# Kernel tuning notes

Hardware: AMD Instinct MI355X
Metric: run time of the kernel (lower is better)

## Reference

```python
import jax, jax.numpy as jnp
import numpy as np

TILE = 128
NEG = -1e10


def rotate_half(x):
    half = x.shape[-1] // 2
    return jnp.concatenate([-x[..., half:], x[..., :half]], axis=-1)


def setup_inputs() -> dict:
    key = jax.random.key(0)
    ks = jax.random.split(key, 7)
    B, S, E, H, D, K = 1, 4096, 2048, 16, 128, 8
    T = S // TILE
    x = jax.random.normal(ks[0], (B, S, E), jnp.float32)
    wq = jax.random.normal(ks[1], (E, H * D), jnp.float32) * 0.02
    wk = jax.random.normal(ks[2], (E, H * D), jnp.float32) * 0.02
    wv = jax.random.normal(ks[3], (E, H * D), jnp.float32) * 0.02
    wo = jax.random.normal(ks[4], (H * D, E), jnp.float32) * 0.02
    rope_angles = jax.random.uniform(ks[5], (S, D // 2), jnp.float32)
    anchor_indices = jax.random.randint(ks[6], (B, H, T, K), 0, T).astype(jnp.int32)
    return {"x": x, "wq": wq, "wk": wk, "wv": wv, "wo": wo,
            "rope_angles": rope_angles, "anchor_indices": anchor_indices}


def reference(x, wq, wk, wv, wo, rope_angles, anchor_indices):
    B, S, E = x.shape
    D = rope_angles.shape[1] * 2          # head_dim
    H = wq.shape[1] // D                  # num_heads
    T = S // TILE                         # num_tiles
    sm_scale = 1.0 / jnp.sqrt(jnp.float32(D))

    # QKV projections -> [B, H, S, D]
    def proj(w):
        return (x @ w).reshape(B, S, H, D).transpose(0, 2, 1, 3).astype(jnp.float32)
    q, k, v = proj(wq), proj(wk), proj(wv)

    # RoPE (half-split / rotate_half format)
    cos = jnp.cos(rope_angles)[None, None]   # [1,1,S,D/2]
    sin = jnp.sin(rope_angles)[None, None]
    cos_f = jnp.concatenate([cos, cos], axis=-1)
    sin_f = jnp.concatenate([sin, sin], axis=-1)
    q = q * cos_f + rotate_half(q) * sin_f
    k = k * cos_f + rotate_half(k) * sin_f

    # Tile selection: anchor tiles + local (diagonal) tile -> [B,H,T,K+1]
    local = jnp.broadcast_to(jnp.arange(T, dtype=jnp.int32)[None, None, :, None], (B, H, T, 1))
    tile_sel = jnp.concatenate([anchor_indices, local], axis=-1)
    L = tile_sel.shape[-1] * TILE            # sparse_len
    token_idx = tile_sel[..., None] * TILE + jnp.arange(TILE, dtype=jnp.int32)[None, None, None, None, :]
    flat_idx = jnp.clip(token_idx.reshape(B, H, T, L), 0, S - 1)  # [B,H,T,L]

    # Gather selected KV tiles: [B,H,T,L,D]
    def gather(kv):
        return jnp.take_along_axis(kv, flat_idx.reshape(B, H, T * L, 1), axis=2).reshape(B, H, T, L, D)
    k_sp, v_sp = gather(k), gather(v)

    # Block-sparse attention per query tile
    q_t = q.reshape(B, H, T, TILE, D)
    logits = jnp.einsum('bhtqd,bhtkd->bhtqk', q_t, k_sp) * sm_scale
    q_pos = jnp.arange(S).reshape(T, TILE)
    future = flat_idx[:, :, :, None, :] > q_pos[None, None, :, :, None]  # causal mask on gathered keys
    logits = jnp.where(future, NEG, logits)
    w = jax.nn.softmax(logits, axis=-1)
    all_masked = jnp.all(future, axis=-1, keepdims=True)
    w = jnp.where(all_masked, 0.0, w)
    w = jnp.where(jnp.isnan(w), 0.0, w)
    out = jnp.einsum('bhtqk,bhtkd->bhtqd', w, v_sp)

    out = out.reshape(B, H, S, D).transpose(0, 2, 1, 3).reshape(B, S, H * D)
    return out @ wo
```

## Files before the change

kernel.cpp:

```cpp
#include <hip/hip_runtime.h>
#include <stdint.h>

typedef unsigned short u16;
typedef unsigned int u32;

#define S_LEN 4096
#define EMB 2048
#define NH 16
#define HD 128
#define HDTOT 2048
#define T_TILES 32
#define KANCH 8
#define SM_SCALE 0.088388347648318447f

typedef __bf16 bf16x8 __attribute__((ext_vector_type(8)));
typedef float f32x4 __attribute__((ext_vector_type(4)));

typedef const __attribute__((address_space(1))) u32 ga_u32;
typedef __attribute__((address_space(3))) u32 lds_u32;

__device__ __forceinline__ u16 f2bf(float f) {
  u32 b = __builtin_bit_cast(u32, f);
  b = (b + 0x7FFFu + ((b >> 16) & 1u)) >> 16;
  return (u16)b;
}
__device__ __forceinline__ float bf2f(u16 u) {
  return __builtin_bit_cast(float, ((u32)u) << 16);
}
__device__ __forceinline__ f32x4 mfma16(bf16x8 a, bf16x8 b, f32x4 c) {
  return __builtin_amdgcn_mfma_f32_16x16x32_bf16(a, b, c, 0, 0, 0);
}

#define ASM_LGKM0 do { asm volatile("s_waitcnt lgkmcnt(0)" ::: "memory"); \
                       __builtin_amdgcn_sched_barrier(0); } while (0)
#define ASM_VMC(n) do { asm volatile("s_waitcnt vmcnt(" #n ")" ::: "memory"); \
                        __builtin_amdgcn_sched_barrier(0); } while (0)

__global__ __launch_bounds__(256) void k_sincos(const float* __restrict__ ang,
                                                float2* __restrict__ tab) {
  int i = blockIdx.x * 256 + threadIdx.x;
  float a = ang[i];
  float s, c;
  __sincosf(a, &s, &c);
  tab[i] = make_float2(c, s);
}

__global__ __launch_bounds__(256) void k_convert_x(const float* __restrict__ x,
                                                   u16* __restrict__ xb) {
  int i = (blockIdx.x * 256 + threadIdx.x) * 4;
  float4 v = *(const float4*)(x + i);
  ushort4 o;
  o.x = f2bf(v.x); o.y = f2bf(v.y); o.z = f2bf(v.z); o.w = f2bf(v.w);
  *(ushort4*)(xb + i) = o;
}

__global__ __launch_bounds__(256) void k_transpose_w(
    const float* __restrict__ w0, const float* __restrict__ w1,
    const float* __restrict__ w2, const float* __restrict__ w3,
    u16* __restrict__ o0, u16* __restrict__ o1,
    u16* __restrict__ o2, u16* __restrict__ o3) {
  const float* w; u16* o;
  if (blockIdx.z == 0)      { w = w0; o = o0; }
  else if (blockIdx.z == 1) { w = w1; o = o1; }
  else if (blockIdx.z == 2) { w = w2; o = o2; }
  else                      { w = w3; o = o3; }
  __shared__ float tile[64][68];
  int n0 = blockIdx.x * 64, k0 = blockIdx.y * 64;
  int tid = threadIdx.x;
  int r = tid >> 4, cq = (tid & 15) << 2;
  for (int p = 0; p < 4; ++p) {
    float4 v = *(const float4*)(w + (size_t)(k0 + r + p * 16) * EMB + n0 + cq);
    tile[r + p * 16][cq + 0] = v.x;
    tile[r + p * 16][cq + 1] = v.y;
    tile[r + p * 16][cq + 2] = v.z;
    tile[r + p * 16][cq + 3] = v.w;
  }
  __syncthreads();
  for (int p = 0; p < 4; ++p) {
    int rn = r + p * 16;
    ushort4 u;
    u.x = f2bf(tile[cq + 0][rn]);
    u.y = f2bf(tile[cq + 1][rn]);
    u.z = f2bf(tile[cq + 2][rn]);
    u.w = f2bf(tile[cq + 3][rn]);
    *(ushort4*)(o + (size_t)(n0 + rn) * EMB + k0 + cq) = u;
  }
}

__global__ __launch_bounds__(256) void k_transpose_v(const u16* __restrict__ v,
                                                     u16* __restrict__ vt) {
  __shared__ u16 tile[64][72];
  int n0 = blockIdx.x * 64, s0 = blockIdx.y * 64;
  int tid = threadIdx.x;
  int r = tid >> 4, cq = (tid & 15) << 2;
  for (int p = 0; p < 4; ++p) {
    ushort4 u = *(const ushort4*)(v + (size_t)(s0 + r + p * 16) * HDTOT + n0 + cq);
    tile[r + p * 16][cq + 0] = u.x;
    tile[r + p * 16][cq + 1] = u.y;
    tile[r + p * 16][cq + 2] = u.z;
    tile[r + p * 16][cq + 3] = u.w;
  }
  __syncthreads();
  for (int p = 0; p < 4; ++p) {
    int rn = r + p * 16;
    ushort4 o;
    o.x = tile[cq + 0][rn];
    o.y = tile[cq + 1][rn];
    o.z = tile[cq + 2][rn];
    o.w = tile[cq + 3][rn];
    *(ushort4*)(vt + (size_t)(n0 + rn) * S_LEN + s0 + cq) = o;
  }
}

template <bool BF16OUT>
__device__ __forceinline__ void gemm_body(const u16* __restrict__ A,
                                          const u16* __restrict__ Bt,
                                          void* __restrict__ Cv,
                                          int N, int K, int m0, int n0,
                                          u16* As, u16* Bs) {
  const int tid = threadIdx.x;
  const int lane = tid & 63, wave = tid >> 6;
  const int quad = lane >> 4, l16 = lane & 15;
  const int wm = (wave >> 1) * 64, wn = (wave & 1) * 64;
  f32x4 acc[4][4] = {};

  const int flat0 = wave * 1024 + lane * 16;
  for (int kt = 0; kt < K; kt += 32) {
    for (int half = 0; half < 2; ++half) {
      int flat = flat0 + half * 4096;
      int row = flat >> 6, colb = flat & 63;
      const char* ga = (const char*)A + ((size_t)(m0 + row) * K + kt) * 2 + colb;
      const char* gb = (const char*)Bt + ((size_t)(n0 + row) * K + kt) * 2 + colb;
      int loff = wave * 1024 + half * 4096;
      __builtin_amdgcn_global_load_lds((ga_u32*)ga, (lds_u32*)((char*)As + loff), 16, 0, 0);
      __builtin_amdgcn_global_load_lds((ga_u32*)gb, (lds_u32*)((char*)Bs + loff), 16, 0, 0);
    }
    __syncthreads();
    bf16x8 af[4], bfr[4];
    for (int mt = 0; mt < 4; ++mt)
      af[mt] = *(const bf16x8*)(As + (wm + mt * 16 + l16) * 32 + quad * 8);
    for (int nt = 0; nt < 4; ++nt)
      bfr[nt] = *(const bf16x8*)(Bs + (wn + nt * 16 + l16) * 32 + quad * 8);
    for (int mt = 0; mt < 4; ++mt)
      for (int nt = 0; nt < 4; ++nt)
        acc[mt][nt] = mfma16(af[mt], bfr[nt], acc[mt][nt]);
    __syncthreads();
  }
  for (int mt = 0; mt < 4; ++mt) {
    int row = m0 + wm + mt * 16 + quad * 4;
    for (int nt = 0; nt < 4; ++nt) {
      int col = n0 + wn + nt * 16 + l16;
      for (int r = 0; r < 4; ++r) {
        if (BF16OUT)
          ((u16*)Cv)[(size_t)(row + r) * N + col] = f2bf(acc[mt][nt][r]);
        else
          ((float*)Cv)[(size_t)(row + r) * N + col] = acc[mt][nt][r];
      }
    }
  }
}

template <bool BF16OUT>
__global__ __launch_bounds__(256) void k_gemm(const u16* __restrict__ A,
                                              const u16* __restrict__ Bt,
                                              void* __restrict__ Cv,
                                              int N, int K) {
  __shared__ __align__(16) u16 As[128 * 32];
  __shared__ __align__(16) u16 Bs[128 * 32];
  gemm_body<BF16OUT>(A, Bt, Cv, N, K, blockIdx.y * 128, blockIdx.x * 128, As, Bs);
}

__global__ __launch_bounds__(512, 2) void k_gemm256_qkv(
    const u16* __restrict__ A, const u16* __restrict__ Bt,
    u16* __restrict__ q, u16* __restrict__ k, u16* __restrict__ v,
    const float2* __restrict__ cssn) {
  __shared__ __align__(16) u16 lds[65536];
  int flat = blockIdx.y * 24 + blockIdx.x;
  flat = (flat & 7) * 48 + (flat >> 3);
  const int bx = flat % 24, by = flat / 24;
  const int m0 = by * 256;
  const int n0g = bx * 256;
  u16* out = (bx < 8) ? q : ((bx < 16) ? k : v);
  const int ncol0 = (bx & 7) * 256;

  const int tid = threadIdx.x;
  const int lane = tid & 63, wave = tid >> 6;
  const int quad = lane >> 4, l16 = lane & 15;
  const int wm = wave >> 2, wn = wave & 3;
  const int sw0 = (quad ^ (l16 & 7)) * 8, sw1 = ((quad ^ (l16 & 7)) ^ 4) * 8;

  size_t soff[2];
#pragma unroll
  for (int p = 0; p < 2; ++p) {
    int fl = p * 8192 + tid * 16;
    int row = fl >> 7;
    int gsw = ((fl >> 4) & 7) ^ (row & 7);
    soff[p] = (size_t)row * 4096 + (size_t)(gsw * 16);
  }
  const char* aBase = (const char*)A + (size_t)m0 * 4096;
  const char* bBase = (const char*)Bt + (size_t)n0g * 4096;
  const int dstW = wave * 1024;

  auto stA = [&](int buf, int half, int kt) {
#pragma unroll
    for (int p = 0; p < 2; ++p)
      __builtin_amdgcn_global_load_lds(
          (ga_u32*)(aBase + (size_t)half * 524288 + (size_t)kt * 128 + soff[p]),
          (lds_u32*)((char*)lds + buf * 32768 + half * 16384 + p * 8192 + dstW),
          16, 0, 0);
  };
  auto stB = [&](int buf, int half, int kt) {
#pragma unroll
    for (int p = 0; p < 2; ++p)
      __builtin_amdgcn_global_load_lds(
          (ga_u32*)(bBase + (size_t)half * 524288 + (size_t)kt * 128 + soff[p]),
          (lds_u32*)((char*)lds + 65536 + buf * 32768 + half * 16384 + p * 8192 + dstW),
          16, 0, 0);
  };
  const u16* aRd = lds + wm * 8192 + l16 * 64;
  const u16* bRd = lds + 32768 + (wn * 16 + l16) * 64;

  f32x4 acc[8][4] = {};

  stB(0, 0, 0); stA(0, 0, 0); stB(0, 1, 0); stA(0, 1, 0);
  stB(1, 0, 1); stA(1, 0, 1);
  ASM_VMC(4);
  __builtin_amdgcn_s_barrier();

  const int NT = EMB / 64;
  for (int j = 0; j < NT; ++j) {
    const int par = j & 1;
    const u16* aT = aRd + par * 16384;
    const u16* bT = bRd + par * 16384;
    bf16x8 af[4][2], blo[2][2], bhi[2][2];
#pragma unroll
    for (int m = 0; m < 4; ++m) {
      af[m][0] = *(const bf16x8*)(aT + m * 1024 + sw0);
      af[m][1] = *(const bf16x8*)(aT + m * 1024 + sw1);
    }
#pragma unroll
    for (int n = 0; n < 2; ++n) {
      blo[n][0] = *(const bf16x8*)(bT + n * 4096 + sw0);
      blo[n][1] = *(const bf16x8*)(bT + n * 4096 + sw1);
    }
    if (j + 1 < NT) stB(1 - par, 1, j + 1);
    __builtin_amdgcn_s_barrier();
    ASM_LGKM0;
    __builtin_amdgcn_s_setprio(1);
#pragma unroll
    for (int m = 0; m < 4; ++m)
#pragma unroll
      for (int n = 0; n < 2; ++n) {
        acc[m][n] = mfma16(af[m][0], blo[n][0], acc[m][n]);
        acc[m][n] = mfma16(af[m][1], blo[n][1], acc[m][n]);
      }
    __builtin_amdgcn_s_setprio(0);
    __builtin_amdgcn_s_barrier();
#pragma unroll
    for (int n = 0; n < 2; ++n) {
      bhi[n][0] = *(const bf16x8*)(bT + (n + 2) * 4096 + sw0);
      bhi[n][1] = *(const bf16x8*)(bT + (n + 2) * 4096 + sw1);
    }
    if (j + 1 < NT) stA(1 - par, 1, j + 1);
    __builtin_amdgcn_s_barrier();
    ASM_LGKM0;
    __builtin_amdgcn_s_setprio(1);
#pragma unroll
    for (int m = 0; m < 4; ++m)
#pragma unroll
      for (int n = 0; n < 2; ++n) {
        acc[m][n + 2] = mfma16(af[m][0], bhi[n][0], acc[m][n + 2]);
        acc[m][n + 2] = mfma16(af[m][1], bhi[n][1], acc[m][n + 2]);
      }
    __builtin_amdgcn_s_setprio(0);
    __builtin_amdgcn_s_barrier();
#pragma unroll
    for (int m = 0; m < 4; ++m) {
      af[m][0] = *(const bf16x8*)(aT + (m + 4) * 1024 + sw0);
      af[m][1] = *(const bf16x8*)(aT + (m + 4) * 1024 + sw1);
    }
    if (j + 2 < NT) stB(par, 0, j + 2);
    __builtin_amdgcn_s_barrier();
    ASM_LGKM0;
    __builtin_amdgcn_s_setprio(1);
#pragma unroll
    for (int m = 0; m < 4; ++m)
#pragma unroll
      for (int n = 0; n < 2; ++n) {
        acc[m + 4][n + 2] = mfma16(af[m][0], bhi[n][0], acc[m + 4][n + 2]);
        acc[m + 4][n + 2] = mfma16(af[m][1], bhi[n][1], acc[m + 4][n + 2]);
      }
    __builtin_amdgcn_s_setprio(0);
    __builtin_amdgcn_s_barrier();
    if (j + 2 < NT) stA(par, 0, j + 2);
    __builtin_amdgcn_s_barrier();
    __builtin_amdgcn_s_setprio(1);
#pragma unroll
    for (int m = 0; m < 4; ++m)
#pragma unroll
      for (int n = 0; n < 2; ++n) {
        acc[m + 4][n] = mfma16(af[m][0], blo[n][0], acc[m + 4][n]);
        acc[m + 4][n] = mfma16(af[m][1], blo[n][1], acc[m + 4][n]);
      }
    __builtin_amdgcn_s_setprio(0);
    if (j == NT - 2) { ASM_VMC(0); } else { ASM_VMC(4); }
    __builtin_amdgcn_s_barrier();
  }

  if (bx < 16) {
    const int dcol = wn * 16 + l16;
#pragma unroll
    for (int m = 0; m < 8; ++m) {
      int srow = m0 + wm * 128 + m * 16 + quad * 4;
#pragma unroll
      for (int r = 0; r < 4; ++r) {
        int s = srow + r;
        float2 cs2 = cssn[s * 64 + dcol];
        u16* op = out + (size_t)s * HDTOT + ncol0 + dcol;
        float lo0 = acc[m][0][r], hi0 = acc[m][1][r];
        op[0]   = f2bf(lo0 * cs2.x - hi0 * cs2.y);
        op[64]  = f2bf(hi0 * cs2.x + lo0 * cs2.y);
        float lo1 = acc[m][2][r], hi1 = acc[m][3][r];
        op[128] = f2bf(lo1 * cs2.x - hi1 * cs2.y);
        op[192] = f2bf(hi1 * cs2.x + lo1 * cs2.y);
      }
    }
  } else {
#pragma unroll
    for (int m = 0; m < 8; ++m) {
      int row = m0 + wm * 128 + m * 16 + quad * 4;
#pragma unroll
      for (int n = 0; n < 4; ++n) {
        int col = ncol0 + (wn + 4 * n) * 16 + l16;
#pragma unroll
        for (int r = 0; r < 4; ++r)
          out[(size_t)(row + r) * HDTOT + col] = f2bf(acc[m][n][r]);
      }
    }
  }
}

__device__ __forceinline__ bf16x8 ldsfrag(const u16* __restrict__ sbuf, int r, int cb) {
  return *(const bf16x8*)(sbuf + r * 128 + (((cb ^ (r & 15)) << 3)));
}
__device__ __forceinline__ bf16x8 ldsfragV(const u16* __restrict__ sbuf, int r, int cb) {
  return *(const bf16x8*)(sbuf + r * 64 + (((cb ^ (r & 7)) << 3)));
}

__global__ __launch_bounds__(512, 4) void k_attn(const u16* __restrict__ q,
                                                 const u16* __restrict__ k,
                                                 const u16* __restrict__ vt,
                                                 const int* __restrict__ anch,
                                                 u16* __restrict__ out) {
  __shared__ __align__(16) u16 bufK[2][64 * 128];
  __shared__ __align__(16) u16 bufV[2][128 * 64];
  __shared__ int s_tj[KANCH + 1];
  __shared__ int s_nv;
  const int i = blockIdx.x;
  const int p2 = (i ^ (i >> 8)) & 1;
  const int c = i >> 1;
  const int t = p2 ? (15 - (c >> 4)) : (16 + (c >> 4));
  const int h = c & 15;
  const int tid = threadIdx.x;
  const int lane = tid & 63, wave = tid >> 6;
  const int quad = lane >> 4, l16 = lane & 15;
  const int wq0 = wave * 16;

  int offK[2], offV[2];
#pragma unroll
  for (int p = 0; p < 2; ++p) {
    int krow = (wave * 2 + p) * 4 + (lane >> 4);
    int kcol = ((lane & 15) ^ (krow & 15)) << 3;
    offK[p] = (krow * HDTOT + kcol) * 2;
    int vrow = (wave * 2 + p) * 8 + (lane >> 3);
    int vcol = ((lane & 7) ^ (vrow & 7)) << 3;
    offV[p] = (vrow * S_LEN + vcol) * 2;
  }

  if (tid == 0) {
    int nv = 0;
    for (int j = 0; j < KANCH; ++j) {
      int tj = anch[((h * T_TILES) + t) * KANCH + j];
      if (tj <= t) s_tj[nv++] = tj;
    }
    s_tj[nv++] = t;
    s_nv = nv;
  }

  {
    const char* gq = (const char*)(q + (size_t)(t * 128) * HDTOT + h * HD);
    char* lq = (char*)bufK + wave * 4096;
#pragma unroll
    for (int p = 0; p < 4; ++p) {
      int qrow = (wave * 4 + p) * 4 + (lane >> 4);
      int qcol = ((lane & 15) ^ (qrow & 15)) << 3;
      __builtin_amdgcn_global_load_lds((ga_u32*)(gq + (qrow * HDTOT + qcol) * 2),
                                       (lds_u32*)(lq + p * 1024), 16, 0, 0);
    }
  }
  __syncthreads();

  bf16x8 qf[4];
#pragma unroll
  for (int ks = 0; ks < 4; ++ks)
    qf[ks] = ldsfrag(&bufK[0][0], wq0 + l16, ks * 4 + quad);

  const int nv2 = 2 * s_nv;
  const char* kh = (const char*)(k + h * HD);
  const char* vh = (const char*)(vt + (size_t)(h * HD) * S_LEN);

  __syncthreads();

  {
    int key0 = s_tj[0] * 128;
    const char* gk = kh + (size_t)key0 * (HDTOT * 2);
    const char* gv = vh + (size_t)key0 * 2;
    char* lk = (char*)bufK[0] + wave * 2048;
    char* lv = (char*)bufV[0] + wave * 2048;
#pragma unroll
    for (int p = 0; p < 2; ++p) {
      __builtin_amdgcn_global_load_lds((ga_u32*)(gk + offK[p]),
                                       (lds_u32*)(lk + p * 1024), 16, 0, 0);
      __builtin_amdgcn_global_load_lds((ga_u32*)(gv + offV[p]),
                                       (lds_u32*)(lv + p * 1024), 16, 0, 0);
    }
  }

  f32x4 oacc[8] = {};
  float m_st = -1e30f, l_st = 0.f;

  for (int it = 0; it < nv2; ++it) {
    const int par = it & 1;
    const u16* K_c = bufK[par];
    const u16* V_c = bufV[par];
    const int tj = s_tj[it >> 1];
    const int half = it & 1;
    const bool diag = (tj == t);

    __syncthreads();

    if (it + 1 < nv2) {
      int inx = it + 1;
      int key0 = s_tj[inx >> 1] * 128 + (inx & 1) * 64;
      const char* gk = kh + (size_t)key0 * (HDTOT * 2);
      const char* gv = vh + (size_t)key0 * 2;
      char* lk = (char*)bufK[1 - par] + wave * 2048;
      char* lv = (char*)bufV[1 - par] + wave * 2048;
#pragma unroll
      for (int p = 0; p < 2; ++p) {
        __builtin_amdgcn_global_load_lds((ga_u32*)(gk + offK[p]),
                                         (lds_u32*)(lk + p * 1024), 16, 0, 0);
        __builtin_amdgcn_global_load_lds((ga_u32*)(gv + offV[p]),
                                         (lds_u32*)(lv + p * 1024), 16, 0, 0);
      }
    }

    f32x4 sacc[4] = {};
#pragma unroll
    for (int ks = 0; ks < 4; ++ks)
#pragma unroll
      for (int a = 0; a < 4; ++a) {
        bf16x8 kf = ldsfrag(K_c, a * 16 + l16, ks * 4 + quad);
        sacc[a] = mfma16(kf, qf[ks], sacc[a]);
      }

    u32 pl[4], ph[4];
    float alpha;
    {
      const int qr = wq0 + l16;
      const int kb = half * 64;
      float rmax = -1e30f;
#pragma unroll
      for (int a = 0; a < 4; ++a) {
        f32x4 s4 = sacc[a];
#pragma unroll
        for (int r = 0; r < 4; ++r) {
          float sv = s4[r] * SM_SCALE;
          if (diag && (kb + a * 16 + quad * 4 + r > qr)) sv = -1e30f;
          s4[r] = sv;
          rmax = fmaxf(rmax, sv);
        }
        sacc[a] = s4;
      }
      rmax = fmaxf(rmax, __shfl_xor(rmax, 16));
      rmax = fmaxf(rmax, __shfl_xor(rmax, 32));
      float mnew = fmaxf(m_st, rmax);
      alpha = __expf(m_st - mnew);
      m_st = mnew;
      float rsum = 0.f;
#pragma unroll
      for (int a = 0; a < 4; ++a) {
        f32x4 s4 = sacc[a];
        float p0 = __expf(s4[0] - mnew);
        float p1 = __expf(s4[1] - mnew);
        float p2 = __expf(s4[2] - mnew);
        float p3 = __expf(s4[3] - mnew);
        rsum += (p0 + p1) + (p2 + p3);
        pl[a] = __builtin_amdgcn_perm(__builtin_bit_cast(u32, p1) + 0x8000u,
                                      __builtin_bit_cast(u32, p0) + 0x8000u,
                                      0x07060302u);
        ph[a] = __builtin_amdgcn_perm(__builtin_bit_cast(u32, p3) + 0x8000u,
                                      __builtin_bit_cast(u32, p2) + 0x8000u,
                                      0x07060302u);
      }
      rsum += __shfl_xor(rsum, 16);
      rsum += __shfl_xor(rsum, 32);
      l_st = l_st * alpha + rsum;
    }

    {
      f32x4 av;
#pragma unroll
      for (int r = 0; r < 4; ++r)
        av[r] = __shfl(alpha, (lane & 48) | (quad * 4 + r));
#pragma unroll
      for (int nt = 0; nt < 8; ++nt) {
        f32x4 o4 = oacc[nt];
        o4[0] *= av[0]; o4[1] *= av[1]; o4[2] *= av[2]; o4[3] *= av[3];
        oacc[nt] = o4;
      }
    }

    const int srcA = ((quad & 1) << 5) + l16;
    const int srcB = srcA + 16;
    const int hi = quad >> 1;
#pragma unroll
    for (int cc = 0; cc < 2; ++cc) {
      u32 x0 = __shfl(pl[2 * cc], srcA), x1 = __shfl(ph[2 * cc], srcA);
      u32 x2 = __shfl(pl[2 * cc], srcB), x3 = __shfl(ph[2 * cc], srcB);
      u32 y0 = __shfl(pl[2 * cc + 1], srcA), y1 = __shfl(ph[2 * cc + 1], srcA);
      u32 y2 = __shfl(pl[2 * cc + 1], srcB), y3 = __shfl(ph[2 * cc + 1], srcB);
      uint4 w;
      w.x = hi ? y0 : x0;
      w.y = hi ? y1 : x1;
      w.z = hi ? y2 : x2;
      w.w = hi ? y3 : x3;
      bf16x8 pa = __builtin_bit_cast(bf16x8, w);
#pragma unroll
      for (int nt = 0; nt < 8; ++nt) {
        bf16x8 vf = ldsfragV(V_c, nt * 16 + l16, cc * 4 + quad);
        oacc[nt] = mfma16(pa, vf, oacc[nt]);
      }
    }
  }

  {
    float linv = 1.0f / l_st;
    f32x4 iv;
#pragma unroll
    for (int r = 0; r < 4; ++r)
      iv[r] = __shfl(linv, (lane & 48) | (quad * 4 + r));
#pragma unroll
    for (int r = 0; r < 4; ++r) {
      size_t srow_o = (size_t)(t * 128 + wq0 + quad * 4 + r);
#pragma unroll
      for (int nt = 0; nt < 8; ++nt)
        out[srow_o * HDTOT + h * HD + nt * 16 + l16] = f2bf(oacc[nt][r] * iv[r]);
    }
  }
}

extern "C" void kernel_launch(void* const* d_in, const int* in_sizes, int n_in,
                              void* d_out, int out_size, void* d_ws, size_t ws_size,
                              hipStream_t stream) {
  const float* x   = (const float*)d_in[0];
  const float* wq  = (const float*)d_in[1];
  const float* wk  = (const float*)d_in[2];
  const float* wv  = (const float*)d_in[3];
  const float* wo  = (const float*)d_in[4];
  const float* ang = (const float*)d_in[5];
  const int* anch  = (const int*)d_in[6];

  char* ws = (char*)d_ws;
  const size_t SZ_SE = (size_t)S_LEN * HDTOT * sizeof(u16);
  const size_t SZ_W  = (size_t)EMB * EMB * sizeof(u16);
  u16* xb   = (u16*)(ws);
  u16* qb   = (u16*)(ws + SZ_SE);
  u16* kb   = (u16*)(ws + 2 * SZ_SE);
  u16* vb   = (u16*)(ws + 3 * SZ_SE);
  u16* vtb  = (u16*)(ws + 4 * SZ_SE);
  u16* attn = (u16*)(ws + 5 * SZ_SE);
  u16* wqT  = (u16*)(ws + 6 * SZ_SE);
  u16* wkT  = (u16*)(ws + 6 * SZ_SE + SZ_W);
  u16* wvT  = (u16*)(ws + 6 * SZ_SE + 2 * SZ_W);
  u16* woT  = (u16*)(ws + 6 * SZ_SE + 3 * SZ_W);

  float2* cssn = (float2*)d_out;

  k_sincos<<<1024, 256, 0, stream>>>(ang, cssn);
  k_convert_x<<<8192, 256, 0, stream>>>(x, xb);
  k_transpose_w<<<dim3(32, 32, 4), 256, 0, stream>>>(wq, wk, wv, wo, wqT, wkT, wvT, woT);
  k_gemm256_qkv<<<dim3(24, 16), 512, 0, stream>>>(xb, wqT, qb, kb, vb, cssn);
  k_transpose_v<<<dim3(32, 64), 256, 0, stream>>>(vb, vtb);
  k_attn<<<dim3(512), 512, 0, stream>>>(qb, kb, vtb, anch, attn);
  k_gemm<false><<<dim3(16, 32), 256, 0, stream>>>(attn, woT, d_out, EMB, HDTOT);
}
```

Measured before the change: 382.2 us.

## Shrink QKV GEMM tile to 128x256 with K-step 32 and higher occupancy

After: 389.3 us. No clear change (+1.9%).

```diff
diff --git a/kernel.cpp b/kernel.cpp
--- a/kernel.cpp
+++ b/kernel.cpp
@@ -170,15 +170,15 @@
   gemm_body<BF16OUT>(A, Bt, Cv, N, K, blockIdx.y * 128, blockIdx.x * 128, As, Bs);
 }
 
-__global__ __launch_bounds__(512, 2) void k_gemm256_qkv(
+__global__ __launch_bounds__(512, 4) void k_gemm_qkv128(
     const u16* __restrict__ A, const u16* __restrict__ Bt,
     u16* __restrict__ q, u16* __restrict__ k, u16* __restrict__ v,
     const float2* __restrict__ cssn) {
-  __shared__ __align__(16) u16 lds[65536];
+  __shared__ __align__(16) u16 lds[24576];
   int flat = blockIdx.y * 24 + blockIdx.x;
-  flat = (flat & 7) * 48 + (flat >> 3);
+  flat = (flat & 7) * 96 + (flat >> 3);
   const int bx = flat % 24, by = flat / 24;
-  const int m0 = by * 256;
+  const int m0 = by * 128;
   const int n0g = bx * 256;
   u16* out = (bx < 8) ? q : ((bx < 16) ? k : v);
   const int ncol0 = (bx & 7) * 256;
@@ -187,131 +187,82 @@
   const int lane = tid & 63, wave = tid >> 6;
   const int quad = lane >> 4, l16 = lane & 15;
   const int wm = wave >> 2, wn = wave & 3;
-  const int sw0 = (quad ^ (l16 & 7)) * 8, sw1 = ((quad ^ (l16 & 7)) ^ 4) * 8;
-
-  size_t soff[2];
-#pragma unroll
-  for (int p = 0; p < 2; ++p) {
-    int fl = p * 8192 + tid * 16;
-    int row = fl >> 7;
-    int gsw = ((fl >> 4) & 7) ^ (row & 7);
-    soff[p] = (size_t)row * 4096 + (size_t)(gsw * 16);
+  const int sw = (quad ^ (l16 & 3)) * 8;
+
+  u32 soffA, soffB1;
+  {
+    int r = tid >> 2, g = tid & 3;
+    soffA = (u32)r * 4096 + (u32)((g ^ (r & 3)) * 16);
+    int r1 = 128 + r;
+    soffB1 = (u32)r1 * 4096 + (u32)((g ^ (r1 & 3)) * 16);
   }
   const char* aBase = (const char*)A + (size_t)m0 * 4096;
   const char* bBase = (const char*)Bt + (size_t)n0g * 4096;
   const int dstW = wave * 1024;
 
-  auto stA = [&](int buf, int half, int kt) {
-#pragma unroll
-    for (int p = 0; p < 2; ++p)
-      __builtin_amdgcn_global_load_lds(
-          (ga_u32*)(aBase + (size_t)half * 524288 + (size_t)kt * 128 + soff[p]),
-          (lds_u32*)((char*)lds + buf * 32768 + half * 16384 + p * 8192 + dstW),
-          16, 0, 0);
+  auto stA = [&](int buf, int kt) {
+    __builtin_amdgcn_global_load_lds(
+        (ga_u32*)(aBase + (size_t)kt * 64 + soffA),
+        (lds_u32*)((char*)lds + buf * 8192 + dstW), 16, 0, 0);
   };
-  auto stB = [&](int buf, int half, int kt) {
-#pragma unroll
-    for (int p = 0; p < 2; ++p)
-      __builtin_amdgcn_global_load_lds(
-          (ga_u32*)(bBase + (size_t)half * 524288 + (size_t)kt * 128 + soff[p]),
-          (lds_u32*)((char*)lds + 65536 + buf * 32768 + half * 16384 + p * 8192 + dstW),
-          16, 0, 0);
+  auto stB = [&](int buf, int kt) {
+    __builtin_amdgcn_global_load_lds(
+        (ga_u32*)(bBase + (size_t)kt * 64 + soffA),
+        (lds_u32*)((char*)lds + 16384 + buf * 16384 + dstW), 16, 0, 0);
+    __builtin_amdgcn_global_load_lds(
+        (ga_u32*)(bBase + (size_t)kt * 64 + soffB1),
+        (lds_u32*)((char*)lds + 16384 + buf * 16384 + 8192 + dstW), 16, 0, 0);
   };
-  const u16* aRd = lds + wm * 8192 + l16 * 64;
-  const u16* bRd = lds + 32768 + (wn * 16 + l16) * 64;
-
-  f32x4 acc[8][4] = {};
-
-  stB(0, 0, 0); stA(0, 0, 0); stB(0, 1, 0); stA(0, 1, 0);
-  stB(1, 0, 1); stA(1, 0, 1);
-  ASM_VMC(4);
+
+  const int aOff = (wm * 64 + l16) * 32 + sw;
+  const int bOff = (wn * 16 + l16) * 32 + sw;
+
+  f32x4 acc[4][4] = {};
+
+  stA(0, 0); stB(0, 0);
+  stA(1, 1); stB(1, 1);
+  ASM_VMC(3);
   __builtin_amdgcn_s_barrier();
 
-  const int NT = EMB / 64;
+  const int NT = EMB / 32;
   for (int j = 0; j < NT; ++j) {
     const int par = j & 1;
-    const u16* aT = aRd + par * 16384;
-    const u16* bT = bRd + par * 16384;
-    bf16x8 af[4][2], blo[2][2], bhi[2][2];
-#pragma unroll
-    for (int m = 0; m < 4; ++m) {
-      af[m][0] = *(const bf16x8*)(aT + m * 1024 + sw0);
-      af[m][1] = *(const bf16x8*)(aT + m * 1024 + sw1);
-    }
-#pragma unroll
-    for (int n = 0; n < 2; ++n) {
-      blo[n][0] = *(const bf16x8*)(bT + n * 4096 + sw0);
-      blo[n][1] = *(const bf16x8*)(bT + n * 4096 + sw1);
-    }
-    if (j + 1 < NT) stB(1 - par, 1, j + 1);
-    __builtin_amdgcn_s_barrier();
+    const u16* aT = lds + par * 4096 + aOff;
+    const u16* bT = lds + 8192 + par * 8192 + bOff;
+    bf16x8 af[4], bfr[4];
+#pragma unroll
+    for (int m = 0; m < 4; ++m)
+      af[m] = *(const bf16x8*)(aT + m * 512);
+#pragma unroll
+    for (int n = 0; n < 4; ++n)
+      bfr[n] = *(const bf16x8*)(bT + n * 2048);
     ASM_LGKM0;
     __builtin_amdgcn_s_setprio(1);
 #pragma unroll
-    for (int m = 0; m < 4; ++m)
-#pragma unroll
-      for (int n = 0; n < 2; ++n) {
-        acc[m][n] = mfma16(af[m][0], blo[n][0], acc[m][n]);
-        acc[m][n] = mfma16(af[m][1], blo[n][1], acc[m][n]);
-      }
+    for (int m = 0; m < 4; ++m) {
+      acc[m][0] = mfma16(af[m], bfr[0], acc[m][0]);
+      acc[m][1] = mfma16(af[m], bfr[1], acc[m][1]);
+    }
     __builtin_amdgcn_s_setprio(0);
     __builtin_amdgcn_s_barrier();
-#pragma unroll
-    for (int n = 0; n < 2; ++n) {
-      bhi[n][0] = *(const bf16x8*)(bT + (n + 2) * 4096 + sw0);
-      bhi[n][1] = *(const bf16x8*)(bT + (n + 2) * 4096 + sw1);
-    }
-    if (j + 1 < NT) stA(1 - par, 1, j + 1);
-    __builtin_amdgcn_s_barrier();
-    ASM_LGKM0;
+    if (j + 2 < NT) { stA(par, j + 2); stB(par, j + 2); }
     __builtin_amdgcn_s_setprio(1);
 #pragma unroll
-    for (int m = 0; m < 4; ++m)
-#pragma unroll
-      for (int n = 0; n < 2; ++n) {
-        acc[m][n + 2] = mfma16(af[m][0], bhi[n][0], acc[m][n + 2]);
-        acc[m][n + 2] = mfma16(af[m][1], bhi[n][1], acc[m][n + 2]);
-      }
+    for (int m = 0; m < 4; ++m) {
+      acc[m][2] = mfma16(af[m], bfr[2], acc[m][2]);
+      acc[m][3] = mfma16(af[m], bfr[3], acc[m][3]);
+    }
     __builtin_amdgcn_s_setprio(0);
-    __builtin_amdgcn_s_barrier();
-#pragma unroll
-    for (int m = 0; m < 4; ++m) {
-      af[m][0] = *(const bf16x8*)(aT + (m + 4) * 1024 + sw0);
-      af[m][1] = *(const bf16x8*)(aT + (m + 4) * 1024 + sw1);
-    }
-    if (j + 2 < NT) stB(par, 0, j + 2);
-    __builtin_amdgcn_s_barrier();
-    ASM_LGKM0;
-    __builtin_amdgcn_s_setprio(1);
-#pragma unroll
-    for (int m = 0; m < 4; ++m)
-#pragma unroll
-      for (int n = 0; n < 2; ++n) {
-        acc[m + 4][n + 2] = mfma16(af[m][0], bhi[n][0], acc[m + 4][n + 2]);
-        acc[m + 4][n + 2] = mfma16(af[m][1], bhi[n][1], acc[m + 4][n + 2]);
-      }
-    __builtin_amdgcn_s_setprio(0);
-    __builtin_amdgcn_s_barrier();
-    if (j + 2 < NT) stA(par, 0, j + 2);
-    __builtin_amdgcn_s_barrier();
-    __builtin_amdgcn_s_setprio(1);
-#pragma unroll
-    for (int m = 0; m < 4; ++m)
-#pragma unroll
-      for (int n = 0; n < 2; ++n) {
-        acc[m + 4][n] = mfma16(af[m][0], blo[n][0], acc[m + 4][n]);
-        acc[m + 4][n] = mfma16(af[m][1], blo[n][1], acc[m + 4][n]);
-      }
-    __builtin_amdgcn_s_setprio(0);
-    if (j == NT - 2) { ASM_VMC(0); } else { ASM_VMC(4); }
-    __builtin_amdgcn_s_barrier();
+    if (j < NT - 2) { ASM_VMC(3); }
+    else if (j == NT - 2) { ASM_VMC(0); }
+    if (j < NT - 1) __builtin_amdgcn_s_barrier();
   }
 
   if (bx < 16) {
     const int dcol = wn * 16 + l16;
 #pragma unroll
-    for (int m = 0; m < 8; ++m) {
-      int srow = m0 + wm * 128 + m * 16 + quad * 4;
+    for (int m = 0; m < 4; ++m) {
+      int srow = m0 + wm * 64 + m * 16 + quad * 4;
 #pragma unroll
       for (int r = 0; r < 4; ++r) {
         int s = srow + r;
@@ -327,8 +278,8 @@
     }
   } else {
 #pragma unroll
-    for (int m = 0; m < 8; ++m) {
-      int row = m0 + wm * 128 + m * 16 + quad * 4;
+    for (int m = 0; m < 4; ++m) {
+      int row = m0 + wm * 64 + m * 16 + quad * 4;
 #pragma unroll
       for (int n = 0; n < 4; ++n) {
         int col = ncol0 + (wn + 4 * n) * 16 + l16;
@@ -590,7 +541,7 @@
   k_sincos<<<1024, 256, 0, stream>>>(ang, cssn);
   k_convert_x<<<8192, 256, 0, stream>>>(x, xb);
   k_transpose_w<<<dim3(32, 32, 4), 256, 0, stream>>>(wq, wk, wv, wo, wqT, wkT, wvT, woT);
-  k_gemm256_qkv<<<dim3(24, 16), 512, 0, stream>>>(xb, wqT, qb, kb, vb, cssn);
+  k_gemm_qkv128<<<dim3(24, 32), 512, 0, stream>>>(xb, wqT, qb, kb, vb, cssn);
   k_transpose_v<<<dim3(32, 64), 256, 0, stream>>>(vb, vtb);
   k_attn<<<dim3(512), 512, 0, stream>>>(qb, kb, vtb, anch, attn);
   k_gemm<false><<<dim3(16, 32), 256, 0, stream>>>(attn, woT, d_out, EMB, HDTOT);
```

## Process two query sub-tiles per wave in attention and swizzle GEMM LDS

Applied to the files above, without the earlier changes.

Result: no change. 382.5 us (+0.1%).

```diff
diff --git a/kernel.cpp b/kernel.cpp
--- a/kernel.cpp
+++ b/kernel.cpp
@@ -122,13 +122,16 @@
   const int lane = tid & 63, wave = tid >> 6;
   const int quad = lane >> 4, l16 = lane & 15;
   const int wm = (wave >> 1) * 64, wn = (wave & 1) * 64;
+  const int sw = (quad ^ (l16 & 3) ^ ((l16 >> 2) & 3)) * 8;
   f32x4 acc[4][4] = {};
 
   const int flat0 = wave * 1024 + lane * 16;
   for (int kt = 0; kt < K; kt += 32) {
     for (int half = 0; half < 2; ++half) {
       int flat = flat0 + half * 4096;
-      int row = flat >> 6, colb = flat & 63;
+      int row = flat >> 6;
+      int gl = (flat >> 4) & 3;
+      int colb = ((gl ^ (row & 3) ^ ((row >> 2) & 3)) << 4);
       const char* ga = (const char*)A + ((size_t)(m0 + row) * K + kt) * 2 + colb;
       const char* gb = (const char*)Bt + ((size_t)(n0 + row) * K + kt) * 2 + colb;
       int loff = wave * 1024 + half * 4096;
@@ -138,9 +141,9 @@
     __syncthreads();
     bf16x8 af[4], bfr[4];
     for (int mt = 0; mt < 4; ++mt)
-      af[mt] = *(const bf16x8*)(As + (wm + mt * 16 + l16) * 32 + quad * 8);
+      af[mt] = *(const bf16x8*)(As + (wm + mt * 16 + l16) * 32 + sw);
     for (int nt = 0; nt < 4; ++nt)
-      bfr[nt] = *(const bf16x8*)(Bs + (wn + nt * 16 + l16) * 32 + quad * 8);
+      bfr[nt] = *(const bf16x8*)(Bs + (wn + nt * 16 + l16) * 32 + sw);
     for (int mt = 0; mt < 4; ++mt)
       for (int nt = 0; nt < 4; ++nt)
         acc[mt][nt] = mfma16(af[mt], bfr[nt], acc[mt][nt]);
@@ -347,7 +350,7 @@
   return *(const bf16x8*)(sbuf + r * 64 + (((cb ^ (r & 7)) << 3)));
 }
 
-__global__ __launch_bounds__(512, 4) void k_attn(const u16* __restrict__ q,
+__global__ __launch_bounds__(256, 2) void k_attn(const u16* __restrict__ q,
                                                  const u16* __restrict__ k,
                                                  const u16* __restrict__ vt,
                                                  const int* __restrict__ anch,
@@ -364,15 +367,15 @@
   const int tid = threadIdx.x;
   const int lane = tid & 63, wave = tid >> 6;
   const int quad = lane >> 4, l16 = lane & 15;
-  const int wq0 = wave * 16;
-
-  int offK[2], offV[2];
-#pragma unroll
-  for (int p = 0; p < 2; ++p) {
-    int krow = (wave * 2 + p) * 4 + (lane >> 4);
+  const int wq0 = wave * 32;
+
+  int offK[4], offV[4];
+#pragma unroll
+  for (int p = 0; p < 4; ++p) {
+    int krow = (wave * 4 + p) * 4 + (lane >> 4);
     int kcol = ((lane & 15) ^ (krow & 15)) << 3;
     offK[p] = (krow * HDTOT + kcol) * 2;
-    int vrow = (wave * 2 + p) * 8 + (lane >> 3);
+    int vrow = (wave * 4 + p) * 8 + (lane >> 3);
     int vcol = ((lane & 7) ^ (vrow & 7)) << 3;
     offV[p] = (vrow * S_LEN + vcol) * 2;
   }
@@ -389,10 +392,10 @@
 
   {
     const char* gq = (const char*)(q + (size_t)(t * 128) * HDTOT + h * HD);
-    char* lq = (char*)bufK + wave * 4096;
-#pragma unroll
-    for (int p = 0; p < 4; ++p) {
-      int qrow = (wave * 4 + p) * 4 + (lane >> 4);
+    char* lq = (char*)bufK + wave * 8192;
+#pragma unroll
+    for (int p = 0; p < 8; ++p) {
+      int qrow = (wave * 8 + p) * 4 + (lane >> 4);
       int qcol = ((lane & 15) ^ (qrow & 15)) << 3;
       __builtin_amdgcn_global_load_lds((ga_u32*)(gq + (qrow * HDTOT + qcol) * 2),
                                        (lds_u32*)(lq + p * 1024), 16, 0, 0);
@@ -400,10 +403,12 @@
   }
   __syncthreads();
 
-  bf16x8 qf[4];
-#pragma unroll
-  for (int ks = 0; ks < 4; ++ks)
-    qf[ks] = ldsfrag(&bufK[0][0], wq0 + l16, ks * 4 + quad);
+  bf16x8 qf[2][4];
+#pragma unroll
+  for (int qh = 0; qh < 2; ++qh)
+#pragma unroll
+    for (int ks = 0; ks < 4; ++ks)
+      qf[qh][ks] = ldsfrag(&bufK[0][0], wq0 + qh * 16 + l16, ks * 4 + quad);
 
   const int nv2 = 2 * s_nv;
   const char* kh = (const char*)(k + h * HD);
@@ -415,10 +420,10 @@
     int key0 = s_tj[0] * 128;
     const char* gk = kh + (size_t)key0 * (HDTOT * 2);
     const char* gv = vh + (size_t)key0 * 2;
-    char* lk = (char*)bufK[0] + wave * 2048;
-    char* lv = (char*)bufV[0] + wave * 2048;
-#pragma unroll
-    for (int p = 0; p < 2; ++p) {
+    char* lk = (char*)bufK[0] + wave * 4096;
+    char* lv = (char*)bufV[0] + wave * 4096;
+#pragma unroll
+    for (int p = 0; p < 4; ++p) {
       __builtin_amdgcn_global_load_lds((ga_u32*)(gk + offK[p]),
                                        (lds_u32*)(lk + p * 1024), 16, 0, 0);
       __builtin_amdgcn_global_load_lds((ga_u32*)(gv + offV[p]),
@@ -426,8 +431,9 @@
     }
   }
 
-  f32x4 oacc[8] = {};
-  float m_st = -1e30f, l_st = 0.f;
+  f32x4 oacc[2][8] = {};
+  float m_st[2] = {-1e30f, -1e30f};
+  float l_st[2] = {0.f, 0.f};
 
   for (int it = 0; it < nv2; ++it) {
     const int par = it & 1;
@@ -444,10 +450,10 @@
       int key0 = s_tj[inx >> 1] * 128 + (inx & 1) * 64;
       const char* gk = kh + (size_t)key0 * (HDTOT * 2);
       const char* gv = vh + (size_t)key0 * 2;
-      char* lk = (char*)bufK[1 - par] + wave * 2048;
-      char* lv = (char*)bufV[1 - par] + wave * 2048;
-#pragma unroll
-      for (int p = 0; p < 2; ++p) {
+      char* lk = (char*)bufK[1 - par] + wave * 4096;
+      char* lv = (char*)bufV[1 - par] + wave * 4096;
+#pragma unroll
+      for (int p = 0; p < 4; ++p) {
         __builtin_amdgcn_global_load_lds((ga_u32*)(gk + offK[p]),
                                          (lds_u32*)(lk + p * 1024), 16, 0, 0);
         __builtin_amdgcn_global_load_lds((ga_u32*)(gv + offV[p]),
@@ -455,24 +461,28 @@
       }
     }
 
-    f32x4 sacc[4] = {};
+    f32x4 sacc[2][4] = {};
+    __builtin_amdgcn_s_setprio(1);
 #pragma unroll
     for (int ks = 0; ks < 4; ++ks)
 #pragma unroll
       for (int a = 0; a < 4; ++a) {
         bf16x8 kf = ldsfrag(K_c, a * 16 + l16, ks * 4 + quad);
-        sacc[a] = mfma16(kf, qf[ks], sacc[a]);
-      }
-
-    u32 pl[4], ph[4];
-    float alpha;
-    {
-      const int qr = wq0 + l16;
+        sacc[0][a] = mfma16(kf, qf[0][ks], sacc[0][a]);
+        sacc[1][a] = mfma16(kf, qf[1][ks], sacc[1][a]);
+      }
+    __builtin_amdgcn_s_setprio(0);
+
+    u32 pl[2][4], ph[2][4];
+    float alpha[2];
+#pragma unroll
+    for (int qh = 0; qh < 2; ++qh) {
+      const int qr = wq0 + qh * 16 + l16;
       const int kb = half * 64;
       float rmax = -1e30f;
 #pragma unroll
       for (int a = 0; a < 4; ++a) {
-        f32x4 s4 = sacc[a];
+        f32x4 s4 = sacc[qh][a];
 #pragma unroll
         for (int r = 0; r < 4; ++r) {
           float sv = s4[r] * SM_SCALE;
@@ -480,44 +490,45 @@
           s4[r] = sv;
           rmax = fmaxf(rmax, sv);
         }
-        sacc[a] = s4;
+        sacc[qh][a] = s4;
       }
       rmax = fmaxf(rmax, __shfl_xor(rmax, 16));
       rmax = fmaxf(rmax, __shfl_xor(rmax, 32));
-      float mnew = fmaxf(m_st, rmax);
-      alpha = __expf(m_st - mnew);
-      m_st = mnew;
+      float mnew = fmaxf(m_st[qh], rmax);
+      alpha[qh] = __expf(m_st[qh] - mnew);
+      m_st[qh] = mnew;
       float rsum = 0.f;
 #pragma unroll
       for (int a = 0; a < 4; ++a) {
-        f32x4 s4 = sacc[a];
-        float p0 = __expf(s4[0] - mnew);
-        float p1 = __expf(s4[1] - mnew);
-        float p2 = __expf(s4[2] - mnew);
-        float p3 = __expf(s4[3] - mnew);
-        rsum += (p0 + p1) + (p2 + p3);
-        pl[a] = __builtin_amdgcn_perm(__builtin_bit_cast(u32, p1) + 0x8000u,
-                                      __builtin_bit_cast(u32, p0) + 0x8000u,
-                                      0x07060302u);
-        ph[a] = __builtin_amdgcn_perm(__builtin_bit_cast(u32, p3) + 0x8000u,
-                                      __builtin_bit_cast(u32, p2) + 0x8000u,
-                                      0x07060302u);
+        f32x4 s4 = sacc[qh][a];
+        float e0 = __expf(s4[0] - mnew);
+        float e1 = __expf(s4[1] - mnew);
+        float e2 = __expf(s4[2] - mnew);
+        float e3 = __expf(s4[3] - mnew);
+        rsum += (e0 + e1) + (e2 + e3);
+        pl[qh][a] = __builtin_amdgcn_perm(__builtin_bit_cast(u32, e1) + 0x8000u,
+                                          __builtin_bit_cast(u32, e0) + 0x8000u,
+                                          0x07060302u);
+        ph[qh][a] = __builtin_amdgcn_perm(__builtin_bit_cast(u32, e3) + 0x8000u,
+                                          __builtin_bit_cast(u32, e2) + 0x8000u,
+                                          0x07060302u);
       }
       rsum += __shfl_xor(rsum, 16);
       rsum += __shfl_xor(rsum, 32);
-      l_st = l_st * alpha + rsum;
-    }
-
-    {
+      l_st[qh] = l_st[qh] * alpha[qh] + rsum;
+    }
+
+#pragma unroll
+    for (int qh = 0; qh < 2; ++qh) {
       f32x4 av;
 #pragma unroll
       for (int r = 0; r < 4; ++r)
-        av[r] = __shfl(alpha, (lane & 48) | (quad * 4 + r));
+        av[r] = __shfl(alpha[qh], (lane & 48) | (quad * 4 + r));
 #pragma unroll
       for (int nt = 0; nt < 8; ++nt) {
-        f32x4 o4 = oacc[nt];
+        f32x4 o4 = oacc[qh][nt];
         o4[0] *= av[0]; o4[1] *= av[1]; o4[2] *= av[2]; o4[3] *= av[3];
-        oacc[nt] = o4;
+        oacc[qh][nt] = o4;
       }
     }
 
@@ -526,36 +537,44 @@
     const int hi = quad >> 1;
 #pragma unroll
     for (int cc = 0; cc < 2; ++cc) {
-      u32 x0 = __shfl(pl[2 * cc], srcA), x1 = __shfl(ph[2 * cc], srcA);
-      u32 x2 = __shfl(pl[2 * cc], srcB), x3 = __shfl(ph[2 * cc], srcB);
-      u32 y0 = __shfl(pl[2 * cc + 1], srcA), y1 = __shfl(ph[2 * cc + 1], srcA);
-      u32 y2 = __shfl(pl[2 * cc + 1], srcB), y3 = __shfl(ph[2 * cc + 1], srcB);
-      uint4 w;
-      w.x = hi ? y0 : x0;
-      w.y = hi ? y1 : x1;
-      w.z = hi ? y2 : x2;
-      w.w = hi ? y3 : x3;
-      bf16x8 pa = __builtin_bit_cast(bf16x8, w);
+      bf16x8 pa[2];
+#pragma unroll
+      for (int qh = 0; qh < 2; ++qh) {
+        u32 x0 = __shfl(pl[qh][2 * cc], srcA), x1 = __shfl(ph[qh][2 * cc], srcA);
+        u32 x2 = __shfl(pl[qh][2 * cc], srcB), x3 = __shfl(ph[qh][2 * cc], srcB);
+        u32 y0 = __shfl(pl[qh][2 * cc + 1], srcA), y1 = __shfl(ph[qh][2 * cc + 1], srcA);
+        u32 y2 = __shfl(pl[qh][2 * cc + 1], srcB), y3 = __shfl(ph[qh][2 * cc + 1], srcB);
+        uint4 w;
+        w.x = hi ? y0 : x0;
+        w.y = hi ? y1 : x1;
+        w.z = hi ? y2 : x2;
+        w.w = hi ? y3 : x3;
+        pa[qh] = __builtin_bit_cast(bf16x8, w);
+      }
+      __builtin_amdgcn_s_setprio(1);
 #pragma unroll
       for (int nt = 0; nt < 8; ++nt) {
         bf16x8 vf = ldsfragV(V_c, nt * 16 + l16, cc * 4 + quad);
-        oacc[nt] = mfma16(pa, vf, oacc[nt]);
-      }
-    }
-  }
-
-  {
-    float linv = 1.0f / l_st;
+        oacc[0][nt] = mfma16(pa[0], vf, oacc[0][nt]);
+        oacc[1][nt] = mfma16(pa[1], vf, oacc[1][nt]);
+      }
+      __builtin_amdgcn_s_setprio(0);
+    }
+  }
+
+#pragma unroll
+  for (int qh = 0; qh < 2; ++qh) {
+    float linv = 1.0f / l_st[qh];
     f32x4 iv;
 #pragma unroll
     for (int r = 0; r < 4; ++r)
       iv[r] = __shfl(linv, (lane & 48) | (quad * 4 + r));
 #pragma unroll
     for (int r = 0; r < 4; ++r) {
-      size_t srow_o = (size_t)(t * 128 + wq0 + quad * 4 + r);
+      size_t srow_o = (size_t)(t * 128 + wq0 + qh * 16 + quad * 4 + r);
 #pragma unroll
       for (int nt = 0; nt < 8; ++nt)
-        out[srow_o * HDTOT + h * HD + nt * 16 + l16] = f2bf(oacc[nt][r] * iv[r]);
+        out[srow_o * HDTOT + h * HD + nt * 16 + l16] = f2bf(oacc[qh][nt][r] * iv[r]);
     }
   }
 }
@@ -592,6 +611,6 @@
   k_transpose_w<<<dim3(32, 32, 4), 256, 0, stream>>>(wq, wk, wv, wo, wqT, wkT, wvT, woT);
   k_gemm256_qkv<<<dim3(24, 16), 512, 0, stream>>>(xb, wqT, qb, kb, vb, cssn);
   k_transpose_v<<<dim3(32, 64), 256, 0, stream>>>(vb, vtb);
-  k_attn<<<dim3(512), 512, 0, stream>>>(qb, kb, vtb, anch, attn);
+  k_attn<<<dim3(512), 256, 0, stream>>>(qb, kb, vtb, anch, attn);
   k_gemm<false><<<dim3(16, 32), 256, 0, stream>>>(attn, woT, d_out, EMB, HDTOT);
 }
```
